# Kernel tuning notes

Hardware: AMD Instinct MI355X
Metric: run time of the kernel (lower is better)

Reference implementation:

```python
import jax, jax.numpy as jnp
import numpy as np
import math

B, L, D, H = 2, 2048, 1024, 16
DH = D // H
TAU = 1.0
EPS_LN = 1e-12


def neural_sort(scores, tau=TAU):
    # scores: (B, n) -> soft permutation P_hat: (B, n, n)
    s = scores[..., None]                                   # (B,n,1)
    A = jnp.abs(s - jnp.swapaxes(s, 1, 2))                  # (B,n,n) pairwise |s_i - s_j|
    Bsum = jnp.sum(A, axis=-1, keepdims=True)               # row sums == A @ ones(n,n) columns
    n = scores.shape[-1]
    scaling = (n + 1 - 2 * (jnp.arange(n) + 1)).astype(scores.dtype)  # (n,)
    C = s * scaling[None, None, :]                          # (B,n,n)
    P_max = jnp.swapaxes(C - Bsum, 1, 2)
    return jax.nn.softmax(P_max / tau, axis=-1)


def euler_transform(v, delta, b_euler, log_scale, is_query):
    # v: (B,L,D); soft-sort channels, polar decompose, rotate, recompose
    Bv, Lv, Dv = v.shape
    scores = v.mean(axis=1)                                 # (B,D)
    P = neural_sort(scores)                                 # (B,D,D)
    v_sorted = jnp.einsum('bij,blj->bli', P, v)             # permute channel dim
    r, p = v_sorted[..., ::2], v_sorted[..., 1::2]          # (B,L,D/2)
    lam = jnp.sqrt(r * r + p * p + 1e-6)
    lam_d = jax.lax.stop_gradient(lam)
    theta = jnp.arctan2(p / lam_d, r / lam_d)
    theta = theta * delta
    if is_query:
        theta = theta + b_euler
    lam = lam * jnp.exp(jnp.clip(log_scale, -5.0, 5.0))
    out = jnp.stack([lam * jnp.cos(theta), lam * jnp.sin(theta)], axis=-1)
    return out.reshape(Bv, Lv, Dv)


def layer_norm(x, gamma, beta, eps=EPS_LN):
    mu = x.mean(axis=-1, keepdims=True)
    var = ((x - mu) ** 2).mean(axis=-1, keepdims=True)
    return (x - mu) / jnp.sqrt(var + eps) * gamma + beta


def forward(input_tensor, Wq, bq, Wk, bk, Wv, bv, Wd, bd, gamma, beta, delta, b_euler, log_scale):
    q = input_tensor @ Wq.T + bq
    k = input_tensor @ Wk.T + bk
    v = input_tensor @ Wv.T + bv
    q = euler_transform(q, delta, b_euler, log_scale, is_query=True)
    k = euler_transform(k, delta, b_euler, log_scale, is_query=False)
    def heads(x):
        return x.reshape(B, L, H, DH).transpose(0, 2, 1, 3)  # (B,H,L,DH)
    qh, kh, vh = heads(q), heads(k), heads(v)
    scores = jnp.einsum('bhqd,bhkd->bhqk', qh, kh) / math.sqrt(DH)
    probs = jax.nn.softmax(scores, axis=-1)                 # dropout off (eval)
    ctx = jnp.einsum('bhqk,bhkd->bhqd', probs, vh)
    ctx = ctx.transpose(0, 2, 1, 3).reshape(B, L, D)
    hidden = ctx @ Wd.T + bd
    return layer_norm(hidden + input_tensor, gamma, beta)


def setup_inputs() -> dict:
    key = jax.random.key(0)
    ks = jax.random.split(key, 16)
    s = 1.0 / math.sqrt(D)
    return {
        'input_tensor': jax.random.normal(ks[0], (B, L, D), jnp.float32),
        'Wq': jax.random.normal(ks[1], (D, D), jnp.float32) * s,
        'bq': jnp.zeros((D,), jnp.float32),
        'Wk': jax.random.normal(ks[2], (D, D), jnp.float32) * s,
        'bk': jnp.zeros((D,), jnp.float32),
        'Wv': jax.random.normal(ks[3], (D, D), jnp.float32) * s,
        'bv': jnp.zeros((D,), jnp.float32),
        'Wd': jax.random.normal(ks[4], (D, D), jnp.float32) * s,
        'bd': jnp.zeros((D,), jnp.float32),
        'gamma': jnp.ones((D,), jnp.float32),
        'beta': jnp.zeros((D,), jnp.float32),
        'delta': jnp.full((1, 1, D // 2), 0.1, jnp.float32),
        'b_euler': jnp.zeros((1, 1, D // 2), jnp.float32),
        'log_scale': jnp.zeros((1, 1, D // 2), jnp.float32),
    }


def reference(input_tensor, Wq, bq, Wk, bk, Wv, bv, Wd, bd, gamma, beta, delta, b_euler, log_scale):
    return forward(input_tensor, Wq, bq, Wk, bk, Wv, bv, Wd, bd, gamma, beta, delta, b_euler, log_scale)
```

## Files before the change

### kernel.cpp

```cpp
#include <hip/hip_runtime.h>


typedef unsigned short bf16_t;
typedef short frag_ab __attribute__((ext_vector_type(8)));
typedef float frag_cd __attribute__((ext_vector_type(4)));

#define BB 2
#define LL 2048
#define DD 1024
#define HH 16
#define DH 64

#define QSCALE 0.18033688f
#define EOFF  -17.3123404907f

__device__ __forceinline__ float b2f(bf16_t u) {
  union { unsigned int i; float f; } c; c.i = ((unsigned int)u) << 16; return c.f;
}
__device__ __forceinline__ bf16_t f2b(float f) {
  union { float f; unsigned int i; } c; c.f = f;
  unsigned int r = c.i + 0x7fffu + ((c.i >> 16) & 1u);
  return (bf16_t)(r >> 16);
}
__device__ __forceinline__ unsigned int fbits(float f) {
  union { float f; unsigned int i; } c; c.f = f; return c.i;
}
__device__ __forceinline__ float waveMax(float v) {
#pragma unroll
  for (int m = 32; m > 0; m >>= 1) v = fmaxf(v, __shfl_xor(v, m));
  return v;
}
__device__ __forceinline__ float waveSum(float v) {
#pragma unroll
  for (int m = 32; m > 0; m >>= 1) v += __shfl_xor(v, m);
  return v;
}

__device__ __forceinline__ void gll16(const bf16_t* g, bf16_t* l) {
  __builtin_amdgcn_global_load_lds(
      (const __attribute__((address_space(1))) void*)g,
      (__attribute__((address_space(3))) void*)l, 16, 0, 0);
}

__device__ __forceinline__ frag_ab ld_tile(const bf16_t* base, int row, int chunk) {
  return *(const frag_ab*)((const char*)base + (row << 7) + (((chunk ^ row) & 7) << 4));
}

__global__ __launch_bounds__(256) void prep_cast(const float* __restrict__ X,
                                                 const float* __restrict__ Wv,
                                                 const float* __restrict__ Wd,
                                                 bf16_t* __restrict__ Xb,
                                                 bf16_t* __restrict__ Wvb,
                                                 bf16_t* __restrict__ Wdb,
                                                 float* __restrict__ xmean) {
  const int bid = blockIdx.x;
  if (bid == 6144) {
    if (threadIdx.x < 256)
      for (int i = threadIdx.x; i < BB * DD; i += 256) xmean[i] = 0.f;
    return;
  }
  const float* in;
  bf16_t* out;
  int i;
  if (bid < 4096)      { in = X;  out = Xb;  i = bid * 256 + threadIdx.x; }
  else if (bid < 5120) { in = Wv; out = Wvb; i = (bid - 4096) * 256 + threadIdx.x; }
  else                 { in = Wd; out = Wdb; i = (bid - 5120) * 256 + threadIdx.x; }
  float4 v = ((const float4*)in)[i];
  ushort4 o;
  o.x = f2b(v.x); o.y = f2b(v.y); o.z = f2b(v.z); o.w = f2b(v.w);
  ((ushort4*)out)[i] = o;
}

__global__ __launch_bounds__(256) void cast_transpose_w(const float* __restrict__ Wq,
                                                        const float* __restrict__ Wk,
                                                        bf16_t* __restrict__ WqT,
                                                        bf16_t* __restrict__ WkT) {
  const float* W = blockIdx.z ? Wk : Wq;
  bf16_t* WT = blockIdx.z ? WkT : WqT;
  __shared__ bf16_t T[64][72];
  const int i0 = blockIdx.x * 64, m0 = blockIdx.y * 64;
  const int tid = threadIdx.x;
#pragma unroll
  for (int it = 0; it < 4; ++it) {
    const int idx = tid + it * 256;
    const int r = idx >> 4, c4 = (idx & 15) * 4;
    float4 v = *(const float4*)&W[(size_t)(i0 + r) * DD + m0 + c4];
    T[c4 + 0][r] = f2b(v.x);
    T[c4 + 1][r] = f2b(v.y);
    T[c4 + 2][r] = f2b(v.z);
    T[c4 + 3][r] = f2b(v.w);
  }
  __syncthreads();
#pragma unroll
  for (int it = 0; it < 2; ++it) {
    const int idx = tid + it * 256;
    const int r = idx >> 3, seg = idx & 7;
    *(uint4*)&WT[(size_t)(m0 + r) * DD + i0 + seg * 8] = *(const uint4*)&T[r][seg * 8];
  }
}

struct GemmB { const bf16_t* A; const bf16_t* Bm; const float* bias; float* Cf; bf16_t* Cb; };
struct GemmArgs { GemmB gb[6]; };

__global__ __launch_bounds__(256) void gemm128(GemmArgs ga, int M, int N, int K) {
  const GemmB g = ga.gb[blockIdx.z];
  const int bm = blockIdx.y * 128, bn = blockIdx.x * 128;
  __shared__ bf16_t As[128][32];
  __shared__ bf16_t Bs[128][32];
  bf16_t* As_f = &As[0][0];
  bf16_t* Bs_f = &Bs[0][0];
  const int tid = threadIdx.x;
  const int lane = tid & 63, w = tid >> 6;
  const int quad = lane >> 4, l16 = lane & 15;
  const int wm = (w >> 1) * 64, wn = (w & 1) * 64;
  const int wbase = w << 9;

  frag_cd acc[4][4];
#pragma unroll
  for (int i = 0; i < 4; ++i)
#pragma unroll
    for (int j = 0; j < 4; ++j)
#pragma unroll
      for (int r = 0; r < 4; ++r) acc[i][j][r] = 0.f;

  const int r0 = tid >> 2, s0 = (tid & 3) * 8;
  const int r1 = (tid + 256) >> 2, s1 = ((tid + 256) & 3) * 8;
  const size_t aoff0 = (size_t)(bm + r0) * K + s0;
  const size_t aoff1 = (size_t)(bm + r1) * K + s1;
  const size_t boff0 = (size_t)(bn + r0) * K + s0;
  const size_t boff1 = (size_t)(bn + r1) * K + s1;

  for (int k0 = 0; k0 < K; k0 += 32) {
    __syncthreads();
    gll16(g.A + aoff0 + k0, As_f + wbase);
    gll16(g.A + aoff1 + k0, As_f + 2048 + wbase);
    gll16(g.Bm + boff0 + k0, Bs_f + wbase);
    gll16(g.Bm + boff1 + k0, Bs_f + 2048 + wbase);
    __syncthreads();
    frag_ab af[4], bfr[4];
#pragma unroll
    for (int i = 0; i < 4; ++i) {
      af[i]  = *(const frag_ab*)&As[wm + i * 16 + l16][quad * 8];
      bfr[i] = *(const frag_ab*)&Bs[wn + i * 16 + l16][quad * 8];
    }
#pragma unroll
    for (int i = 0; i < 4; ++i)
#pragma unroll
      for (int j = 0; j < 4; ++j)
        acc[i][j] = __builtin_amdgcn_mfma_f32_16x16x32_bf16(af[i], bfr[j], acc[i][j], 0, 0, 0);
  }

#pragma unroll
  for (int i = 0; i < 4; ++i) {
#pragma unroll
    for (int r = 0; r < 4; ++r) {
      const int row = bm + wm + i * 16 + quad * 4 + r;
#pragma unroll
      for (int j = 0; j < 4; ++j) {
        const int col = bn + wn + j * 16 + l16;
        float v = acc[i][j][r];
        if (g.bias) v += g.bias[col];
        if (g.Cf) g.Cf[(size_t)row * N + col] = v;
        if (g.Cb) g.Cb[(size_t)row * N + col] = f2b(v);
      }
    }
  }
}

__global__ __launch_bounds__(256) void gemm64x64(GemmArgs ga, int M, int N, int K) {
  const GemmB g = ga.gb[blockIdx.z];
  const int bm = blockIdx.y * 64, bn = blockIdx.x * 64;
  __shared__ bf16_t As[64][32];
  __shared__ bf16_t Bs[64][32];
  bf16_t* As_f = &As[0][0];
  bf16_t* Bs_f = &Bs[0][0];
  const int tid = threadIdx.x;
  const int lane = tid & 63, w = tid >> 6;
  const int quad = lane >> 4, l16 = lane & 15;
  const int wm = (w >> 1) * 32, wn = (w & 1) * 32;
  const int wbase = w << 9;

  frag_cd acc[2][2];
#pragma unroll
  for (int i = 0; i < 2; ++i)
#pragma unroll
    for (int j = 0; j < 2; ++j)
#pragma unroll
      for (int r = 0; r < 4; ++r) acc[i][j][r] = 0.f;

  const int r0 = tid >> 2, s0 = (tid & 3) * 8;
  const size_t aoff0 = (size_t)(bm + r0) * K + s0;
  const size_t boff0 = (size_t)(bn + r0) * K + s0;

  for (int k0 = 0; k0 < K; k0 += 32) {
    __syncthreads();
    gll16(g.A + aoff0 + k0, As_f + wbase);
    gll16(g.Bm + boff0 + k0, Bs_f + wbase);
    __syncthreads();
    frag_ab af[2], bfr[2];
#pragma unroll
    for (int i = 0; i < 2; ++i) {
      af[i]  = *(const frag_ab*)&As[wm + i * 16 + l16][quad * 8];
      bfr[i] = *(const frag_ab*)&Bs[wn + i * 16 + l16][quad * 8];
    }
#pragma unroll
    for (int i = 0; i < 2; ++i)
#pragma unroll
      for (int j = 0; j < 2; ++j)
        acc[i][j] = __builtin_amdgcn_mfma_f32_16x16x32_bf16(af[i], bfr[j], acc[i][j], 0, 0, 0);
  }

#pragma unroll
  for (int i = 0; i < 2; ++i) {
#pragma unroll
    for (int r = 0; r < 4; ++r) {
      const int row = bm + wm + i * 16 + quad * 4 + r;
#pragma unroll
      for (int j = 0; j < 2; ++j) {
        const int col = bn + wn + j * 16 + l16;
        float v = acc[i][j][r];
        if (g.bias) v += g.bias[col];
        if (g.Cf) g.Cf[(size_t)row * N + col] = v;
        if (g.Cb) g.Cb[(size_t)row * N + col] = f2b(v);
      }
    }
  }
}

__global__ __launch_bounds__(256) void xmean_kernel(const float* __restrict__ X,
                                                    float* __restrict__ xmean) {
  const int d = blockIdx.x * 256 + threadIdx.x;
  const int b = blockIdx.z;
  const int l0 = blockIdx.y * 64;
  float s = 0.f;
  for (int l = l0; l < l0 + 64; ++l)
    s += X[((size_t)b * LL + l) * DD + d];
  atomicAdd(&xmean[b * DD + d], s * (1.f / (float)LL));
}

__global__ __launch_bounds__(256) void scores_gemm(const float* __restrict__ xmean,
                                                   const float* __restrict__ Wq,
                                                   const float* __restrict__ bq,
                                                   const float* __restrict__ Wk,
                                                   const float* __restrict__ bk,
                                                   float* __restrict__ scores) {
  const int w = threadIdx.x >> 6, lane = threadIdx.x & 63;
  const int idx = blockIdx.x * 4 + w;
  const int t = idx >> 11, b = (idx >> 10) & 1, i = idx & 1023;
  const float* W = t ? Wk : Wq;
  const float* bias = t ? bk : bq;
  const float* xm = xmean + b * DD;
  float sum = 0.f;
#pragma unroll
  for (int k = 0; k < 4; ++k) {
    float4 wv = *(const float4*)&W[(size_t)i * DD + k * 256 + lane * 4];
    float4 xv = *(const float4*)&xm[k * 256 + lane * 4];
    sum += wv.x * xv.x + wv.y * xv.y + wv.z * xv.z + wv.w * xv.w;
  }
  sum = waveSum(sum);
  if (lane == 0) scores[idx] = sum + bias[i];
}

__global__ __launch_bounds__(256) void bsum_kernel(const float* __restrict__ scores,
                                                   float* __restrict__ bsum) {
  __shared__ float sc[DD];
  const int z = blockIdx.x, jb = blockIdx.y, tid = threadIdx.x;
#pragma unroll
  for (int s = 0; s < 4; ++s) sc[tid + s * 256] = scores[z * DD + tid + s * 256];
  __syncthreads();
  const int j = jb * 256 + tid;
  const float si = sc[j];
  float s = 0.f;
  for (int m = 0; m < DD; m += 4) {
    float4 v = *(const float4*)&sc[m];
    s += fabsf(si - v.x) + fabsf(si - v.y) + fabsf(si - v.z) + fabsf(si - v.w);
  }
  bsum[z * DD + j] = s;
}

__global__ __launch_bounds__(256) void p_kernel(const float* __restrict__ scores,
                                                const float* __restrict__ bsum,
                                                const float* __restrict__ bq,
                                                const float* __restrict__ bk,
                                                bf16_t* __restrict__ Pq,
                                                bf16_t* __restrict__ Pk,
                                                float* __restrict__ bias4) {
  const int i = blockIdx.x;
  const int z = blockIdx.y;
  const int t = z >> 1, b = z & 1;
  const float* sc = scores + z * DD;
  const float* bs = bsum + z * DD;
  const float* bias = t ? bk : bq;
  const float scal = 1023.f - 2.f * (float)i;
  const int tid = threadIdx.x;
  __shared__ float redA[4], redB[4], redC[4];

  float lg[4], bb[4];
  float mx = -1e30f;
#pragma unroll
  for (int s = 0; s < 4; ++s) {
    const int j = tid + s * 256;
    lg[s] = sc[j] * scal - bs[j];
    bb[s] = bias[j];
    mx = fmaxf(mx, lg[s]);
  }
  mx = waveMax(mx);
  if ((tid & 63) == 0) redA[tid >> 6] = mx;
  __syncthreads();
  const float M = fmaxf(fmaxf(redA[0], redA[1]), fmaxf(redA[2], redA[3]));
  float sum = 0.f, dot = 0.f;
#pragma unroll
  for (int s = 0; s < 4; ++s) {
    lg[s] = __expf(lg[s] - M);
    sum += lg[s];
    dot += lg[s] * bb[s];
  }
  sum = waveSum(sum); dot = waveSum(dot);
  if ((tid & 63) == 0) { redB[tid >> 6] = sum; redC[tid >> 6] = dot; }
  __syncthreads();
  const float inv = 1.f / (redB[0] + redB[1] + redB[2] + redB[3]);
  bf16_t* P = (t ? Pk : Pq) + ((size_t)b << 20) + (size_t)i * DD;
#pragma unroll
  for (int s = 0; s < 4; ++s) P[tid + s * 256] = f2b(lg[s] * inv);
  if (tid == 0)
    bias4[t * 2048 + b * 1024 + i] = (redC[0] + redC[1] + redC[2] + redC[3]) * inv;
}

__global__ __launch_bounds__(256) void euler_transv(bf16_t* __restrict__ qs,
                                                    bf16_t* __restrict__ ks,
                                                    const float* __restrict__ delta,
                                                    const float* __restrict__ beul,
                                                    const float* __restrict__ lsc,
                                                    const bf16_t* __restrict__ vb,
                                                    bf16_t* __restrict__ vbT) {
  __shared__ bf16_t T[64][72];
  const int bid = blockIdx.x;
  const int tid = threadIdx.x;
  if (bid < 16384) {
    const int isq = (bid < 8192);
    unsigned int* buf = (unsigned int*)(isq ? qs : ks);
    const int idx = (isq ? bid : bid - 8192) * 256 + tid;
    const int c = idx & 511;
    const size_t n = idx >> 9;
    const unsigned int u = buf[n * 512 + c];
    const float r = b2f((bf16_t)(u & 0xffffu));
    const float p = b2f((bf16_t)(u >> 16));
    float lam = sqrtf(r * r + p * p + 1e-6f);
    float th = atan2f(p, r) * delta[c];
    if (isq) th += beul[c];
    lam *= __expf(fminf(fmaxf(lsc[c], -5.f), 5.f));
    if (isq) lam *= QSCALE;
    float sn, cs;
    __sincosf(th, &sn, &cs);
    buf[n * 512 + c] = ((unsigned int)f2b(lam * sn) << 16) | (unsigned int)f2b(lam * cs);
    return;
  }
  const int tb = bid - 16384;
  const int l0 = (tb & 31) * 64, d0 = ((tb >> 5) & 15) * 64, b = tb >> 9;
  for (int i = tid; i < 512; i += 256) {
    const int r = i >> 3, seg = i & 7;
    uint4 v = *(const uint4*)&vb[((size_t)b * LL + l0 + r) * DD + d0 + seg * 8];
    const bf16_t* vs = (const bf16_t*)&v;
#pragma unroll
    for (int j = 0; j < 8; ++j) T[seg * 8 + j][r] = vs[j];
  }
  __syncthreads();
  for (int i = tid; i < 512; i += 256) {
    const int r = i >> 3, seg = i & 7;
    *(uint4*)&vbT[((size_t)b * DD + d0 + r) * LL + l0 + seg * 8] =
        *(const uint4*)&T[r][seg * 8];
  }
}

__global__ __launch_bounds__(256) void attn_kernel(const bf16_t* __restrict__ Q,
                                                   const bf16_t* __restrict__ Kt,
                                                   const bf16_t* __restrict__ VT,
                                                   bf16_t* __restrict__ O) {
  const int bid = blockIdx.x;
  const int swz = (bid & 7) * 128 + (bid >> 3);
  const int g = swz >> 5;
  const int qt = swz & 31;
  const int b = g >> 4, h = g & 15;
  const int q0 = qt * 64;
  const int tid = threadIdx.x, w = tid >> 6, lane = tid & 63;
  const int quad = lane >> 4, l16 = lane & 15;

  __shared__ bf16_t Ks[2][64 * 64];
  __shared__ bf16_t Vs[2][64 * 64];
  __shared__ bf16_t Ps[64 * 64];

  const size_t base = (size_t)b * LL * DD + (size_t)h * DH;
  const size_t vtb = (size_t)(b * DD + h * DH) * LL;

  frag_ab bq0 = *(const frag_ab*)
      &Q[base + (size_t)(q0 + w * 16 + l16) * DD + quad * 8];
  frag_ab bq1 = *(const frag_ab*)
      &Q[base + (size_t)(q0 + w * 16 + l16) * DD + 32 + quad * 8];

  frag_ab bone;
  {
    const short o = (l16 == 0) ? (short)0x3F80 : (short)0;
#pragma unroll
    for (int j = 0; j < 8; ++j) bone[j] = o;
  }

  frag_cd o_[4], l5;
#pragma unroll
  for (int n = 0; n < 4; ++n)
#pragma unroll
    for (int r = 0; r < 4; ++r) o_[n][r] = 0.f;
#pragma unroll
  for (int r = 0; r < 4; ++r) l5[r] = 0.f;

  const int srow = lane >> 3;
  const int cg = (lane & 7) ^ srow;
  const int rbase = w * 16;

  auto STAGE = [&](int buf, int kt) {
#pragma unroll
    for (int t = 0; t < 2; ++t) {
      const int row = rbase + t * 8 + srow;
      gll16(Kt + base + (size_t)(kt * 64 + row) * DD + cg * 8,
            &Ks[buf][(rbase + t * 8) * 64]);
      gll16(VT + vtb + (size_t)row * LL + kt * 64 + cg * 8,
            &Vs[buf][(rbase + t * 8) * 64]);
    }
  };

  STAGE(0, 0);
  int cur = 0;
  const int NT = LL / 64;
  for (int kt = 0; kt < NT; ++kt) {
    if (kt + 1 < NT) {
      STAGE(cur ^ 1, kt + 1);
      asm volatile("s_waitcnt vmcnt(4)" ::: "memory");
    } else {
      asm volatile("s_waitcnt vmcnt(0)" ::: "memory");
    }
    __builtin_amdgcn_s_barrier();

    const bf16_t* Kb = Ks[cur];
    const bf16_t* Vb = Vs[cur];

    frag_ab ak[4][2];
#pragma unroll
    for (int n = 0; n < 4; ++n) {
      ak[n][0] = ld_tile(Kb, n * 16 + l16, quad);
      ak[n][1] = ld_tile(Kb, n * 16 + l16, 4 + quad);
    }

    const int prow = rbase + l16;
    char* pb = (char*)Ps + prow * 128 + ((quad & 1) << 3);
#pragma unroll
    for (int n = 0; n < 4; ++n) {
      frag_cd z; z[0] = z[1] = z[2] = z[3] = EOFF;
      z = __builtin_amdgcn_mfma_f32_16x16x32_bf16(ak[n][0], bq0, z, 0, 0, 0);
      z = __builtin_amdgcn_mfma_f32_16x16x32_bf16(ak[n][1], bq1, z, 0, 0, 0);
      float p0 = __builtin_amdgcn_exp2f(z[0]);
      float p1 = __builtin_amdgcn_exp2f(z[1]);
      float p2 = __builtin_amdgcn_exp2f(z[2]);
      float p3 = __builtin_amdgcn_exp2f(z[3]);
      unsigned int u01 = __builtin_amdgcn_perm(fbits(p1), fbits(p0), 0x07060302u);
      unsigned int u23 = __builtin_amdgcn_perm(fbits(p3), fbits(p2), 0x07060302u);
      uint2 pk; pk.x = u01; pk.y = u23;
      const int pc = 2 * n + (quad >> 1);
      *(uint2*)(pb + (((pc ^ l16) & 7) << 4)) = pk;
    }

    frag_ab ap0 = ld_tile(Ps, prow, quad);
    frag_ab ap1 = ld_tile(Ps, prow, 4 + quad);

    l5 = __builtin_amdgcn_mfma_f32_16x16x32_bf16(ap0, bone, l5, 0, 0, 0);
    l5 = __builtin_amdgcn_mfma_f32_16x16x32_bf16(ap1, bone, l5, 0, 0, 0);

#pragma unroll
    for (int n = 0; n < 4; ++n) {
      frag_ab bv0 = ld_tile(Vb, n * 16 + l16, quad);
      frag_ab bv1 = ld_tile(Vb, n * 16 + l16, 4 + quad);
      o_[n] = __builtin_amdgcn_mfma_f32_16x16x32_bf16(ap0, bv0, o_[n], 0, 0, 0);
      o_[n] = __builtin_amdgcn_mfma_f32_16x16x32_bf16(ap1, bv1, o_[n], 0, 0, 0);
    }
    __builtin_amdgcn_s_barrier();
    cur ^= 1;
  }

  float lfin[4];
#pragma unroll
  for (int r = 0; r < 4; ++r) lfin[r] = 1.f / __shfl(l5[r], quad << 4);

#pragma unroll
  for (int n = 0; n < 4; ++n)
#pragma unroll
    for (int r = 0; r < 4; ++r) {
      const float v = o_[n][r] * lfin[r];
      O[base + (size_t)(q0 + w * 16 + quad * 4 + r) * DD + n * 16 + l16] = f2b(v);
    }
}

__global__ __launch_bounds__(256) void ln_kernel(const bf16_t* __restrict__ hidden,
                                                 const float* __restrict__ x0,
                                                 const float* __restrict__ gamma,
                                                 const float* __restrict__ beta,
                                                 float* __restrict__ out) {
  const int row = blockIdx.x;
  const int tid = threadIdx.x;
  __shared__ float red1[4], red2[4];
  float v[4];
  float s1 = 0.f, s2 = 0.f;
#pragma unroll
  for (int s = 0; s < 4; ++s) {
    const int c = tid + s * 256;
    const float x = b2f(hidden[(size_t)row * DD + c]) + x0[(size_t)row * DD + c];
    v[s] = x; s1 += x; s2 += x * x;
  }
  s1 = waveSum(s1); s2 = waveSum(s2);
  if ((tid & 63) == 0) { red1[tid >> 6] = s1; red2[tid >> 6] = s2; }
  __syncthreads();
  const float t1 = red1[0] + red1[1] + red1[2] + red1[3];
  const float t2 = red2[0] + red2[1] + red2[2] + red2[3];
  const float mu = t1 * (1.f / DD);
  const float var = t2 * (1.f / DD) - mu * mu;
  const float inv = rsqrtf(var + 1e-12f);
#pragma unroll
  for (int s = 0; s < 4; ++s) {
    const int c = tid + s * 256;
    out[(size_t)row * DD + c] = (v[s] - mu) * inv * gamma[c] + beta[c];
  }
}

extern "C" void kernel_launch(void* const* d_in, const int* in_sizes, int n_in,
                              void* d_out, int out_size, void* d_ws, size_t ws_size,
                              hipStream_t stream) {
  const float* X    = (const float*)d_in[0];
  const float* Wq   = (const float*)d_in[1];
  const float* bq   = (const float*)d_in[2];
  const float* Wk   = (const float*)d_in[3];
  const float* bk   = (const float*)d_in[4];
  const float* Wv   = (const float*)d_in[5];
  const float* bv   = (const float*)d_in[6];
  const float* Wd   = (const float*)d_in[7];
  const float* bd   = (const float*)d_in[8];
  const float* gam  = (const float*)d_in[9];
  const float* bet  = (const float*)d_in[10];
  const float* delt = (const float*)d_in[11];
  const float* beul = (const float*)d_in[12];
  const float* lsc  = (const float*)d_in[13];
  float* out = (float*)d_out;

  char* w = (char*)d_ws;
  const size_t MB = 1024ull * 1024ull;
  bf16_t* Xb  = (bf16_t*)(w + 0 * MB);
  bf16_t* Wvb = (bf16_t*)(w + 8 * MB);
  bf16_t* Wdb = (bf16_t*)(w + 10 * MB);
  bf16_t* WqT = (bf16_t*)(w + 12 * MB);
  bf16_t* WkT = (bf16_t*)(w + 14 * MB);
  bf16_t* Pq  = (bf16_t*)(w + 16 * MB);
  bf16_t* Pk  = (bf16_t*)(w + 20 * MB);
  bf16_t* Wp  = (bf16_t*)(w + 24 * MB);
  bf16_t* vb  = (bf16_t*)(w + 32 * MB);
  bf16_t* qs  = (bf16_t*)(w + 40 * MB);
  bf16_t* ks  = (bf16_t*)(w + 48 * MB);
  bf16_t* vbT = (bf16_t*)(w + 56 * MB);
  bf16_t* ctx = (bf16_t*)(w + 64 * MB);
  bf16_t* hid = (bf16_t*)(w + 24 * MB);
  float*  xmean  = (float*)(w + 72 * MB);
  float*  scores = (float*)(w + 72 * MB + 16384);
  float*  bsum   = (float*)(w + 72 * MB + 32768);
  float*  bias4  = (float*)(w + 72 * MB + 49152);

  const size_t WSZ = (size_t)DD * DD;

  prep_cast<<<dim3(6145), 256, 0, stream>>>(X, Wv, Wd, Xb, Wvb, Wdb, xmean);
  cast_transpose_w<<<dim3(16, 16, 2), 256, 0, stream>>>(Wq, Wk, WqT, WkT);

  xmean_kernel<<<dim3(4, 32, 2), 256, 0, stream>>>(X, xmean);
  scores_gemm<<<dim3(1024), 256, 0, stream>>>(xmean, Wq, bq, Wk, bk, scores);

  bsum_kernel<<<dim3(4, 4), 256, 0, stream>>>(scores, bsum);
  p_kernel<<<dim3(1024, 4), 256, 0, stream>>>(scores, bsum, bq, bk, Pq, Pk, bias4);

  GemmArgs gw = {};
  gw.gb[0] = {Pq,       WqT, nullptr, nullptr, Wp};
  gw.gb[1] = {Pq + WSZ, WqT, nullptr, nullptr, Wp + WSZ};
  gw.gb[2] = {Pk,       WkT, nullptr, nullptr, Wp + 2 * WSZ};
  gw.gb[3] = {Pk + WSZ, WkT, nullptr, nullptr, Wp + 3 * WSZ};
  gemm64x64<<<dim3(16, 16, 4), 256, 0, stream>>>(gw, DD, DD, DD);

  const size_t XHALF = (size_t)LL * DD;
  GemmArgs gs = {};
  gs.gb[0] = {Xb,         Wp,           bias4,        nullptr, qs};
  gs.gb[1] = {Xb + XHALF, Wp + WSZ,     bias4 + 1024, nullptr, qs + XHALF};
  gs.gb[2] = {Xb,         Wp + 2 * WSZ, bias4 + 2048, nullptr, ks};
  gs.gb[3] = {Xb + XHALF, Wp + 3 * WSZ, bias4 + 3072, nullptr, ks + XHALF};
  gs.gb[4] = {Xb,         Wvb,          bv,           nullptr, vb};
  gs.gb[5] = {Xb + XHALF, Wvb,          bv,           nullptr, vb + XHALF};
  gemm128<<<dim3(8, 16, 6), 256, 0, stream>>>(gs, LL, DD, DD);

  euler_transv<<<dim3(17408), 256, 0, stream>>>(qs, ks, delt, beul, lsc, vb, vbT);

  attn_kernel<<<dim3(1024), 256, 0, stream>>>(qs, ks, vbT, ctx);

  GemmArgs g4 = {};
  g4.gb[0] = {ctx, Wdb, bd, nullptr, hid};
  gemm64x64<<<dim3(16, 64, 1), 256, 0, stream>>>(g4, BB * LL, DD, DD);

  ln_kernel<<<dim3(BB * LL), 256, 0, stream>>>(hid, X, gam, bet, out);
}
```

Measured before the change: 297.9 us.

## Use 32x32x16 MFMA in attention with register-resident P and 128-row query tiles

Rewrites the attention inner loop to use 32x32x16 bf16 MFMAs, with each wave owning 32 query rows, so a block covers 128 queries and the grid halves. The exp'd scores are packed straight into A-operand fragments in registers, which removes the LDS round trip for P. To make the register layout line up, the V transpose kernel permutes key order inside each 16-key group. This raises per-wave register pressure and halves block count, which may lower occupancy but doubles K/V reuse per staged tile.

Result: faster. 291.4 us (-2.2%).

```diff
diff --git a/kernel.cpp b/kernel.cpp
--- a/kernel.cpp
+++ b/kernel.cpp
@@ -4,6 +4,7 @@
 typedef unsigned short bf16_t;
 typedef short frag_ab __attribute__((ext_vector_type(8)));
 typedef float frag_cd __attribute__((ext_vector_type(4)));
+typedef float f32x16 __attribute__((ext_vector_type(16)));
 
 #define BB 2
 #define LL 2048
@@ -44,6 +45,15 @@
 
 __device__ __forceinline__ frag_ab ld_tile(const bf16_t* base, int row, int chunk) {
   return *(const frag_ab*)((const char*)base + (row << 7) + (((chunk ^ row) & 7) << 4));
+}
+
+__device__ __forceinline__ frag_ab pack8(const float* p) {
+  union { unsigned int u[4]; frag_ab f; } x;
+  x.u[0] = __builtin_amdgcn_perm(fbits(p[1]), fbits(p[0]), 0x07060302u);
+  x.u[1] = __builtin_amdgcn_perm(fbits(p[3]), fbits(p[2]), 0x07060302u);
+  x.u[2] = __builtin_amdgcn_perm(fbits(p[5]), fbits(p[4]), 0x07060302u);
+  x.u[3] = __builtin_amdgcn_perm(fbits(p[7]), fbits(p[6]), 0x07060302u);
+  return x.f;
 }
 
 __global__ __launch_bounds__(256) void prep_cast(const float* __restrict__ X,
@@ -367,8 +377,11 @@
   __syncthreads();
   for (int i = tid; i < 512; i += 256) {
     const int r = i >> 3, seg = i & 7;
-    *(uint4*)&vbT[((size_t)b * DD + d0 + r) * LL + l0 + seg * 8] =
-        *(const uint4*)&T[r][seg * 8];
+    const int kb = (seg >> 1) * 16 + (seg & 1) * 4;
+    uint2 lo = *(const uint2*)&T[r][kb];
+    uint2 hi2 = *(const uint2*)&T[r][kb + 8];
+    uint4 o; o.x = lo.x; o.y = lo.y; o.z = hi2.x; o.w = hi2.y;
+    *(uint4*)&vbT[((size_t)b * DD + d0 + r) * LL + l0 + seg * 8] = o;
   }
 }
 
@@ -377,40 +390,36 @@
                                                    const bf16_t* __restrict__ VT,
                                                    bf16_t* __restrict__ O) {
   const int bid = blockIdx.x;
-  const int swz = (bid & 7) * 128 + (bid >> 3);
-  const int g = swz >> 5;
-  const int qt = swz & 31;
+  const int swz = (bid & 7) * 64 + (bid >> 3);
+  const int g = swz >> 4;
+  const int qt = swz & 15;
   const int b = g >> 4, h = g & 15;
-  const int q0 = qt * 64;
+  const int q0 = qt * 128;
   const int tid = threadIdx.x, w = tid >> 6, lane = tid & 63;
-  const int quad = lane >> 4, l16 = lane & 15;
+  const int hi = lane >> 5, l31 = lane & 31;
 
   __shared__ bf16_t Ks[2][64 * 64];
   __shared__ bf16_t Vs[2][64 * 64];
-  __shared__ bf16_t Ps[64 * 64];
 
   const size_t base = (size_t)b * LL * DD + (size_t)h * DH;
   const size_t vtb = (size_t)(b * DD + h * DH) * LL;
 
-  frag_ab bq0 = *(const frag_ab*)
-      &Q[base + (size_t)(q0 + w * 16 + l16) * DD + quad * 8];
-  frag_ab bq1 = *(const frag_ab*)
-      &Q[base + (size_t)(q0 + w * 16 + l16) * DD + 32 + quad * 8];
+  frag_ab bq[4];
+#pragma unroll
+  for (int kd = 0; kd < 4; ++kd)
+    bq[kd] = *(const frag_ab*)
+        &Q[base + (size_t)(q0 + w * 32 + l31) * DD + kd * 16 + hi * 8];
 
   frag_ab bone;
   {
-    const short o = (l16 == 0) ? (short)0x3F80 : (short)0;
+    const short o = (l31 == 0) ? (short)0x3F80 : (short)0;
 #pragma unroll
     for (int j = 0; j < 8; ++j) bone[j] = o;
   }
 
-  frag_cd o_[4], l5;
-#pragma unroll
-  for (int n = 0; n < 4; ++n)
-#pragma unroll
-    for (int r = 0; r < 4; ++r) o_[n][r] = 0.f;
-#pragma unroll
-  for (int r = 0; r < 4; ++r) l5[r] = 0.f;
+  f32x16 o_[2], l5;
+#pragma unroll
+  for (int i = 0; i < 16; ++i) { o_[0][i] = 0.f; o_[1][i] = 0.f; l5[i] = 0.f; }
 
   const int srow = lane >> 3;
   const int cg = (lane & 7) ^ srow;
@@ -442,58 +451,56 @@
     const bf16_t* Kb = Ks[cur];
     const bf16_t* Vb = Vs[cur];
 
-    frag_ab ak[4][2];
-#pragma unroll
-    for (int n = 0; n < 4; ++n) {
-      ak[n][0] = ld_tile(Kb, n * 16 + l16, quad);
-      ak[n][1] = ld_tile(Kb, n * 16 + l16, 4 + quad);
-    }
-
-    const int prow = rbase + l16;
-    char* pb = (char*)Ps + prow * 128 + ((quad & 1) << 3);
-#pragma unroll
-    for (int n = 0; n < 4; ++n) {
-      frag_cd z; z[0] = z[1] = z[2] = z[3] = EOFF;
-      z = __builtin_amdgcn_mfma_f32_16x16x32_bf16(ak[n][0], bq0, z, 0, 0, 0);
-      z = __builtin_amdgcn_mfma_f32_16x16x32_bf16(ak[n][1], bq1, z, 0, 0, 0);
-      float p0 = __builtin_amdgcn_exp2f(z[0]);
-      float p1 = __builtin_amdgcn_exp2f(z[1]);
-      float p2 = __builtin_amdgcn_exp2f(z[2]);
-      float p3 = __builtin_amdgcn_exp2f(z[3]);
-      unsigned int u01 = __builtin_amdgcn_perm(fbits(p1), fbits(p0), 0x07060302u);
-      unsigned int u23 = __builtin_amdgcn_perm(fbits(p3), fbits(p2), 0x07060302u);
-      uint2 pk; pk.x = u01; pk.y = u23;
-      const int pc = 2 * n + (quad >> 1);
-      *(uint2*)(pb + (((pc ^ l16) & 7) << 4)) = pk;
-    }
-
-    frag_ab ap0 = ld_tile(Ps, prow, quad);
-    frag_ab ap1 = ld_tile(Ps, prow, 4 + quad);
-
-    l5 = __builtin_amdgcn_mfma_f32_16x16x32_bf16(ap0, bone, l5, 0, 0, 0);
-    l5 = __builtin_amdgcn_mfma_f32_16x16x32_bf16(ap1, bone, l5, 0, 0, 0);
-
-#pragma unroll
-    for (int n = 0; n < 4; ++n) {
-      frag_ab bv0 = ld_tile(Vb, n * 16 + l16, quad);
-      frag_ab bv1 = ld_tile(Vb, n * 16 + l16, 4 + quad);
-      o_[n] = __builtin_amdgcn_mfma_f32_16x16x32_bf16(ap0, bv0, o_[n], 0, 0, 0);
-      o_[n] = __builtin_amdgcn_mfma_f32_16x16x32_bf16(ap1, bv1, o_[n], 0, 0, 0);
-    }
+    frag_ab pa[4];
+#pragma unroll
+    for (int s = 0; s < 2; ++s) {
+      frag_ab ak[4];
+#pragma unroll
+      for (int kd = 0; kd < 4; ++kd)
+        ak[kd] = ld_tile(Kb, s * 32 + l31, kd * 2 + hi);
+      f32x16 z;
+#pragma unroll
+      for (int i = 0; i < 16; ++i) z[i] = EOFF;
+#pragma unroll
+      for (int kd = 0; kd < 4; ++kd)
+        z = __builtin_amdgcn_mfma_f32_32x32x16_bf16(ak[kd], bq[kd], z, 0, 0, 0);
+#pragma unroll
+      for (int t = 0; t < 2; ++t) {
+        float p[8];
+#pragma unroll
+        for (int j = 0; j < 8; ++j) p[j] = __builtin_amdgcn_exp2f(z[t * 8 + j]);
+        pa[s * 2 + t] = pack8(p);
+      }
+    }
+
+#pragma unroll
+    for (int k = 0; k < 4; ++k)
+      l5 = __builtin_amdgcn_mfma_f32_32x32x16_bf16(pa[k], bone, l5, 0, 0, 0);
+
+#pragma unroll
+    for (int dt = 0; dt < 2; ++dt)
+#pragma unroll
+      for (int k = 0; k < 4; ++k) {
+        frag_ab bv = ld_tile(Vb, dt * 32 + l31, k * 2 + hi);
+        o_[dt] = __builtin_amdgcn_mfma_f32_32x32x16_bf16(pa[k], bv, o_[dt], 0, 0, 0);
+      }
+
     __builtin_amdgcn_s_barrier();
     cur ^= 1;
   }
 
-  float lfin[4];
-#pragma unroll
-  for (int r = 0; r < 4; ++r) lfin[r] = 1.f / __shfl(l5[r], quad << 4);
-
-#pragma unroll
-  for (int n = 0; n < 4; ++n)
-#pragma unroll
-    for (int r = 0; r < 4; ++r) {
-      const float v = o_[n][r] * lfin[r];
-      O[base + (size_t)(q0 + w * 16 + quad * 4 + r) * DD + n * 16 + l16] = f2b(v);
+  const int src = (lane >> 5) << 5;
+  float lf[16];
+#pragma unroll
+  for (int r = 0; r < 16; ++r) lf[r] = 1.f / __shfl(l5[r], src);
+
+#pragma unroll
+  for (int dt = 0; dt < 2; ++dt)
+#pragma unroll
+    for (int r = 0; r < 16; ++r) {
+      const int ql = (r & 3) + 8 * (r >> 2) + 4 * hi;
+      O[base + (size_t)(q0 + w * 32 + ql) * DD + dt * 32 + l31] =
+          f2b(o_[dt][r] * lf[r]);
     }
 }
 
@@ -598,7 +605,7 @@
 
   euler_transv<<<dim3(17408), 256, 0, stream>>>(qs, ks, delt, beul, lsc, vb, vbT);
 
-  attn_kernel<<<dim3(1024), 256, 0, stream>>>(qs, ks, vbT, ctx);
+  attn_kernel<<<dim3(512), 256, 0, stream>>>(qs, ks, vbT, ctx);
 
   GemmArgs g4 = {};
   g4.gb[0] = {ctx, Wdb, bd, nullptr, hid};
```
